# Kernel tuning notes

Measured on AMD Instinct MI355X. Metric: run time of the kernel, lower is better.

The kernel has to match this reference:

```python
import jax, jax.numpy as jnp
import numpy as np

N = 20000      # atoms
E = 240000     # edges (avg degree ~12, matches _AVG_DEGREE_MATPES)
C = 128        # sphere_channels
ZMAX = 100     # max_num_elements
NG = 600       # GaussianSmearing(0, cutoff, 600, 2.0)
CUTOFF = 6.0
WIDTH = 2.0    # basis_width_scalar
RESCALE = 12.0 # _AVG_DEGREE_MATPES
LN_EPS = 1e-5
# xyz -> (y,z,x): real-SH component order for l=1, so Wigner D^(1) = P R P^T
P = np.array([[0.,1.,0.],[0.,0.,1.],[1.,0.,0.]], dtype=np.float32)


def _layernorm(x, g, b):
    mu = jnp.mean(x, axis=-1, keepdims=True)
    var = jnp.mean((x - mu) ** 2, axis=-1, keepdims=True)
    return g * (x - mu) * jax.lax.rsqrt(var + LN_EPS) + b


def init_edge_rot_mat(ev):
    # faithful port of init_edge_rot_mat (torch uses .detach())
    ev = jax.lax.stop_gradient(ev)
    dist = jnp.maximum(jnp.linalg.norm(ev, axis=1, keepdims=True), 1e-8)
    nx = ev / dist
    ref = jnp.eye(3, dtype=ev.dtype)[jnp.argmin(jnp.abs(nx), axis=1)]
    nz = jnp.cross(nx, ref)
    nz = nz / jnp.maximum(jnp.linalg.norm(nz, axis=1, keepdims=True), 1e-8)
    ny = jnp.cross(nx, nz)
    ny = ny / jnp.maximum(jnp.linalg.norm(ny, axis=1, keepdims=True), 1e-8)
    # edge_rot_mat_inv has columns [nz, nx, -ny]; rot = inv^T -> rows [nz, nx, -ny]
    return jnp.stack([nz, nx, -ny], axis=1)  # [E,3,3]


def setup_inputs() -> dict:
    key = jax.random.key(0)
    ks = jax.random.split(key, 10)
    s = 0.02
    return {
        'edge_distance_vec': jax.random.normal(ks[0], (E, 3), jnp.float32) * 2.0,
        'sphere_emb': jax.random.normal(ks[1], (ZMAX, C), jnp.float32) * s,
        'src_emb': jax.random.normal(ks[2], (ZMAX, C), jnp.float32) * s,
        'tgt_emb': jax.random.normal(ks[3], (ZMAX, C), jnp.float32) * s,
        'W1': jax.random.normal(ks[4], (NG + 2 * C, C), jnp.float32) * s,
        'b1': jnp.zeros((C,), jnp.float32),
        'g1': jnp.ones((C,), jnp.float32),
        'be1': jnp.zeros((C,), jnp.float32),
        'W2': jax.random.normal(ks[5], (C, C), jnp.float32) * s,
        'b2': jnp.zeros((C,), jnp.float32),
        'g2': jnp.ones((C,), jnp.float32),
        'be2': jnp.zeros((C,), jnp.float32),
        'W3': jax.random.normal(ks[6], (C, 2 * C), jnp.float32) * s,
        'b3': jnp.zeros((2 * C,), jnp.float32),
        'atomic_numbers': jax.random.randint(ks[7], (N,), 0, ZMAX),
        'edge_index': jax.random.randint(ks[8], (2, E), 0, N),
    }


def reference(edge_distance_vec, sphere_emb, src_emb, tgt_emb,
              W1, b1, g1, be1, W2, b2, g2, be2, W3, b3,
              atomic_numbers, edge_index):
    src, dst = edge_index[0], edge_index[1]
    Pm = jnp.asarray(P)
    # per-edge rotation to edge-aligned frame and its l=1 Wigner matrix
    rot = init_edge_rot_mat(edge_distance_vec)               # [E,3,3]
    D1 = jnp.einsum('ij,ejk,lk->eil', Pm, rot, Pm)           # [E,3,3]
    # Gaussian distance expansion (600 basis fns)
    dist = jnp.linalg.norm(edge_distance_vec, axis=1)        # [E]
    offsets = jnp.linspace(0.0, CUTOFF, NG)
    coeff = -0.5 / (WIDTH * (offsets[1] - offsets[0])) ** 2
    gauss = jnp.exp(coeff * (dist[:, None] - offsets[None, :]) ** 2)  # [E,600]
    # edge features: distance basis + source/target atom embeddings
    x_edge = jnp.concatenate(
        [gauss, src_emb[atomic_numbers[src]], tgt_emb[atomic_numbers[dst]]], axis=1)
    # RadialFunction: Linear->LN->SiLU x2, final Linear -> m=0 coefficients
    h = jax.nn.silu(_layernorm(x_edge @ W1 + b1, g1, be1))
    h = jax.nn.silu(_layernorm(h @ W2 + b2, g2, be2))
    m0 = (h @ W3 + b3).reshape(E, 2, C)   # (l=0,m=0) and (l=1,m=0)
    # rotate back to global frame: blockdiag(1, D1)^T applied to (m0[0]; 0, m0[1], 0)
    l0 = m0[:, 0][:, None, :]                                 # [E,1,C]
    l1 = jnp.einsum('ei,ec->eic', D1[:, 1, :], m0[:, 1])      # (D1^T v)_i with v=(0,a,0)
    msg = jnp.concatenate([l0, l1], axis=1)                   # [E,4,C]
    # scatter-sum messages to target nodes, rescale by avg degree
    x_deg = jnp.zeros((N, 4, C), msg.dtype).at[dst].add(msg) / RESCALE
    # node init: atom embedding into l=0 slot, plus edge-degree embedding
    x = x_deg.at[:, 0].add(sphere_emb[atomic_numbers])
    return x
```

## Files before the change

### kernel.cpp

```cpp
#include <hip/hip_runtime.h>
#include <stdint.h>

#define EE 240000
#define NN 20000
#define NB 4096

typedef __attribute__((ext_vector_type(4))) float f32x4;
typedef __attribute__((ext_vector_type(8))) __bf16 bf16x8;
typedef __attribute__((ext_vector_type(8))) short s16x8;

union V8 { s16x8 s; bf16x8 b; uint4 u; };

static constexpr float GC2 =
    (float)((-0.5 / ((12.0 / 599.0) * (12.0 / 599.0))) * 1.4426950408889634);

__device__ __forceinline__ float b2f(unsigned short u) {
    return __uint_as_float(((unsigned)u) << 16);
}
__device__ __forceinline__ unsigned short f2b(float f) {
    unsigned u = __float_as_uint(f);
    return (unsigned short)((u + 0x7fffu + ((u >> 16) & 1u)) >> 16);
}
__device__ __forceinline__ unsigned cvtpk(float lo, float hi) {
    unsigned r;
    asm("v_cvt_pk_bf16_f32 %0, %1, %2" : "=v"(r) : "v"(lo), "v"(hi));
    return r;
}
__device__ __forceinline__ unsigned short ldc(const void* p, int i, bool isb) {
    return isb ? ((const unsigned short*)p)[i] : f2b(((const float*)p)[i]);
}
__device__ __forceinline__ float ldf(const void* p, int i, bool isb) {
    return isb ? b2f(((const unsigned short*)p)[i]) : ((const float*)p)[i];
}
__device__ __forceinline__ bool probe_isb(const void* g1) {
    return ((const unsigned*)g1)[0] != 0x3F800000u;
}

__device__ __forceinline__ int kperm(int p) {
    int wi = p >> 1;
    return ((wi >> 4) << 5) + (wi & 15) + ((p & 1) << 4);
}

#define PREP_PARAMS_TOTAL (114688 + 16384 + 32768 + 2 * 12800 + 6 * 128 + 256)
#define PB ((PREP_PARAMS_TOTAL + 255) / 256)
#define EB ((EE + 255) / 256)

__global__ void prep_all(const void* ev, const int* __restrict__ an,
                         const int* __restrict__ ei,
                         const void* W1, const void* W2, const void* W3,
                         const void* se, const void* te,
                         const void* b1, const void* g1, const void* be1,
                         const void* b2, const void* g2, const void* be2,
                         const void* b3,
                         unsigned short* __restrict__ W1T,
                         unsigned short* __restrict__ W2T,
                         unsigned short* __restrict__ W3T,
                         unsigned short* __restrict__ SE,
                         unsigned short* __restrict__ TE,
                         unsigned short* __restrict__ vecs,
                         uint4* __restrict__ sedge_u, float4* __restrict__ d1_out,
                         int* __restrict__ deg, int* __restrict__ bhist) {
    bool isb = probe_isb(g1);
    int bid = blockIdx.x;
    if (bid < PB) {
        int t = bid * 256 + threadIdx.x;
        if (t < 114688) {
            int j = t & 7, n = (t >> 3) & 127, kb = t >> 10;
            int k = kb * 8 + j;
            unsigned short v = 0;
            if (k < 600) v = ldc(W1, k * 128 + n, isb);
            else if (k >= 608 && k < 864) v = ldc(W1, (k - 8) * 128 + n, isb);
            W1T[t] = v;
            return;
        }
        t -= 114688;
        if (t < 16384) {
            int j = t & 7, n = (t >> 3) & 127, kb = t >> 10;
            W2T[t] = ldc(W2, kperm(kb * 8 + j) * 128 + n, isb);
            return;
        }
        t -= 16384;
        if (t < 32768) {
            int j = t & 7, n = (t >> 3) & 255, kb = t >> 11;
            W3T[t] = ldc(W3, kperm(kb * 8 + j) * 256 + n, isb);
            return;
        }
        t -= 32768;
        if (t < 12800) { SE[t] = ldc(se, t, isb); return; }
        t -= 12800;
        if (t < 12800) { TE[t] = ldc(te, t, isb); return; }
        t -= 12800;
        if (t < 128) { vecs[t] = ldc(b1, t, isb); return; }
        t -= 128;
        if (t < 128) { vecs[128 + t] = ldc(g1, t, isb); return; }
        t -= 128;
        if (t < 128) { vecs[256 + t] = ldc(be1, t, isb); return; }
        t -= 128;
        if (t < 128) { vecs[384 + t] = ldc(b2, t, isb); return; }
        t -= 128;
        if (t < 128) { vecs[512 + t] = ldc(g2, t, isb); return; }
        t -= 128;
        if (t < 128) { vecs[640 + t] = ldc(be2, t, isb); return; }
        t -= 128;
        if (t < 256) { vecs[768 + t] = ldc(b3, t, isb); return; }
        return;
    }
    int e = (bid - PB) * 256 + threadIdx.x;
    if (e >= EE) return;
    float x = ldf(ev, e * 3 + 0, isb);
    float y = ldf(ev, e * 3 + 1, isb);
    float z = ldf(ev, e * 3 + 2, isb);
    float nrm = sqrtf(x * x + y * y + z * z);
    float dc = fmaxf(nrm, 1e-8f);
    float nx0 = x / dc, nx1 = y / dc, nx2 = z / dc;
    float a0 = fabsf(nx0), a1 = fabsf(nx1), a2 = fabsf(nx2);
    int idx = 0; float mv = a0;
    if (a1 < mv) { idx = 1; mv = a1; }
    if (a2 < mv) { idx = 2; }
    float r0 = (idx == 0) ? 1.f : 0.f;
    float r1 = (idx == 1) ? 1.f : 0.f;
    float r2 = (idx == 2) ? 1.f : 0.f;
    float z0 = nx1 * r2 - nx2 * r1;
    float z1 = nx2 * r0 - nx0 * r2;
    float z2 = nx0 * r1 - nx1 * r0;
    float zn = fmaxf(sqrtf(z0 * z0 + z1 * z1 + z2 * z2), 1e-8f);
    z0 /= zn; z1 /= zn; z2 /= zn;
    float y0 = nx1 * z2 - nx2 * z1;
    float y1 = nx2 * z0 - nx0 * z2;
    float y2 = nx0 * z1 - nx1 * z0;
    float yn = fmaxf(sqrtf(y0 * y0 + y1 * y1 + y2 * y2), 1e-8f);
    y0 /= yn; y1 /= yn; y2 /= yn;
    float4 dv; dv.x = -y1; dv.y = -y2; dv.z = -y0; dv.w = 0.f;
    d1_out[e] = dv;
    int zsv = an[ei[e]];
    int dst = ei[EE + e];
    int zdv = an[dst];
    uint4 su;
    su.x = __float_as_uint(nrm);
    su.y = (unsigned)zsv | ((unsigned)zdv << 16);
    su.z = (unsigned)e;
    su.w = 0;
    sedge_u[e] = su;
    atomicAdd(&deg[dst], 1);
    int b = min(NB - 1, (int)(nrm * 512.0f));
    atomicAdd(&bhist[b], 1);
}

__global__ __launch_bounds__(1024) void scan_all(
    const int* __restrict__ deg, const int* __restrict__ bhist,
    int* __restrict__ row_start, int* __restrict__ cursor, int* __restrict__ bcursor) {
    __shared__ int lds[1024];
    int t = threadIdx.x;
    int base = t * 20;
    int loc[20]; int ls = 0;
#pragma unroll
    for (int j = 0; j < 20; ++j) {
        int i = base + j;
        ls += (i < NN) ? deg[i] : 0;
        loc[j] = ls;
    }
    lds[t] = ls; __syncthreads();
    for (int s = 1; s < 1024; s <<= 1) {
        int v = (t >= s) ? lds[t - s] : 0;
        __syncthreads(); lds[t] += v; __syncthreads();
    }
    int off = lds[t] - ls;
#pragma unroll
    for (int j = 0; j < 20; ++j) {
        int i = base + j;
        if (i < NN) {
            row_start[i + 1] = off + loc[j];
            cursor[i] = off + (j ? loc[j - 1] : 0);
        }
    }
    if (t == 0) row_start[0] = 0;
    __syncthreads();
    int b4 = t * 4;
    int l4[4]; int bs = 0;
#pragma unroll
    for (int j = 0; j < 4; ++j) { bs += bhist[b4 + j]; l4[j] = bs; }
    lds[t] = bs; __syncthreads();
    for (int s = 1; s < 1024; s <<= 1) {
        int v = (t >= s) ? lds[t - s] : 0;
        __syncthreads(); lds[t] += v; __syncthreads();
    }
    int boff = lds[t] - bs;
#pragma unroll
    for (int j = 0; j < 4; ++j) bcursor[b4 + j] = boff + (j ? l4[j - 1] : 0);
}

__global__ void fill_sorted(const int* __restrict__ ei,
                            const uint4* __restrict__ sedge_u,
                            const float4* __restrict__ d1v,
                            int* __restrict__ cursor, int* __restrict__ bcursor,
                            uint4* __restrict__ sedge_s, float4* __restrict__ d1s) {
    int e = blockIdx.x * 256 + threadIdx.x;
    if (e >= EE) return;
    uint4 su = sedge_u[e];
    int dst = ei[EE + e];
    int p = atomicAdd(&cursor[dst], 1);
    float d = __uint_as_float(su.x);
    int b = min(NB - 1, (int)(d * 512.0f));
    int sp = atomicAdd(&bcursor[b], 1);
    su.z = (unsigned)p;
    sedge_s[sp] = su;
    d1s[p] = d1v[e];
}

__device__ __forceinline__ void ln_silu(f32x4 (&acc)[8],
                                        const unsigned short* __restrict__ gamma,
                                        const unsigned short* __restrict__ beta,
                                        int i16, int quad,
                                        unsigned short (*ht)[136]) {
    float gm[8], bt[8];
#pragma unroll
    for (int nt = 0; nt < 8; ++nt) {
        gm[nt] = b2f(gamma[nt * 16 + i16]);
        bt[nt] = b2f(beta[nt * 16 + i16]);
    }
#pragma unroll
    for (int r = 0; r < 4; ++r) {
        float s = 0.f, s2 = 0.f;
#pragma unroll
        for (int nt = 0; nt < 8; ++nt) {
            float v = acc[nt][r];
            s += v; s2 += v * v;
        }
#pragma unroll
        for (int m = 1; m < 16; m <<= 1) {
            s += __shfl_xor(s, m);
            s2 += __shfl_xor(s2, m);
        }
        float mu = s * (1.f / 128.f);
        float var = s2 * (1.f / 128.f) - mu * mu;
        float rs = rsqrtf(var + 1e-5f);
        unsigned* wrow = (unsigned*)ht[quad * 4 + r];
#pragma unroll
        for (int ntp = 0; ntp < 4; ++ntp) {
            float zz[2];
#pragma unroll
            for (int h = 0; h < 2; ++h) {
                int nt = 2 * ntp + h;
                float y = gm[nt] * (acc[nt][r] - mu) * rs + bt[nt];
                zz[h] = y * __builtin_amdgcn_rcpf(1.f + exp2f(-1.4426950409f * y));
            }
            wrow[ntp * 16 + i16] = cvtpk(zz[0], zz[1]);
        }
    }
}

template <bool MSG>
__global__ __launch_bounds__(256, 6) void edge_mlp(
    const unsigned short* __restrict__ W1T, const unsigned short* __restrict__ W2T,
    const unsigned short* __restrict__ W3T,
    const unsigned short* __restrict__ SE, const unsigned short* __restrict__ TE,
    const unsigned short* __restrict__ vecs,
    const uint4* __restrict__ sedge,
    const int* __restrict__ ei, const float4* __restrict__ d1v,
    unsigned* __restrict__ msg, float* __restrict__ xacc) {
    __shared__ __align__(16) unsigned short htile_s[4][16][136];
    int tid = threadIdx.x;
    int wave = tid >> 6, lane = tid & 63;
    int i16 = lane & 15, quad = lane >> 4;
    unsigned short (*ht)[136] = htile_s[wave];
    int mbase = blockIdx.x * 64 + wave * 16;

    uint4 s0 = sedge[mbase + i16];
    float dd = __uint_as_float(s0.x);
    int seo = (int)(s0.y & 0xFFFFu) * 128;
    int teo = (int)(s0.y >> 16) * 128;
    int dpz = (int)s0.z;

    float dmn = dd, dmx = dd;
#pragma unroll
    for (int m = 1; m < 64; m <<= 1) {
        dmn = fminf(dmn, __shfl_xor(dmn, m));
        dmx = fmaxf(dmx, __shfl_xor(dmx, m));
    }
    int klo = (int)floorf((dmn - 0.285f) * (599.0f / 6.0f));
    int khi = (int)ceilf((dmx + 0.285f) * (599.0f / 6.0f));
    int ka = min(max(klo, 0) >> 5, 19);
    int kb = min((min(khi, 607) >> 5) + 1, 19);

    f32x4 acc[8];
#pragma unroll
    for (int nt = 0; nt < 8; ++nt) {
        float b = b2f(vecs[nt * 16 + i16]);
#pragma unroll
        for (int q = 0; q < 4; ++q) acc[nt][q] = b;
    }

#pragma unroll 1
    for (int ks = ka; ks < kb; ++ks) {
        int k0 = ks * 32 + quad * 8;
        float e[8];
#pragma unroll
        for (int j = 0; j < 8; ++j) {
            float t = dd - (float)(k0 + j) * (6.0f / 599.0f);
            e[j] = exp2f(GC2 * t * t);
        }
        V8 af;
        af.u.x = cvtpk(e[0], e[1]);
        af.u.y = cvtpk(e[2], e[3]);
        af.u.z = cvtpk(e[4], e[5]);
        af.u.w = cvtpk(e[6], e[7]);
        const unsigned short* w1p = W1T + (((ks * 4 + quad) * 128 + i16) << 3);
#pragma unroll
        for (int nt = 0; nt < 8; ++nt) {
            V8 bf_; bf_.s = *(const s16x8*)(w1p + nt * 128);
            acc[nt] = __builtin_amdgcn_mfma_f32_16x16x32_bf16(af.b, bf_.b, acc[nt], 0, 0, 0);
        }
    }
#pragma unroll 1
    for (int ks = 19; ks < 27; ++ks) {
        int k0 = ks * 32 + quad * 8;
        V8 af;
        if (ks < 23) af.s = *(const s16x8*)(SE + seo + (k0 - 608));
        else         af.s = *(const s16x8*)(TE + teo + (k0 - 736));
        const unsigned short* w1p = W1T + (((ks * 4 + quad) * 128 + i16) << 3);
#pragma unroll
        for (int nt = 0; nt < 8; ++nt) {
            V8 bf_; bf_.s = *(const s16x8*)(w1p + nt * 128);
            acc[nt] = __builtin_amdgcn_mfma_f32_16x16x32_bf16(af.b, bf_.b, acc[nt], 0, 0, 0);
        }
    }
    ln_silu(acc, vecs + 128, vecs + 256, i16, quad, ht);

#pragma unroll
    for (int nt = 0; nt < 8; ++nt) {
        float b = b2f(vecs[384 + nt * 16 + i16]);
#pragma unroll
        for (int q = 0; q < 4; ++q) acc[nt][q] = b;
    }
#pragma unroll 1
    for (int ks = 0; ks < 4; ++ks) {
        int k0 = ks * 32 + quad * 8;
        V8 a0;
        a0.s = *(const s16x8*)&ht[i16][k0];
        const unsigned short* w2p = W2T + (((ks * 4 + quad) * 128 + i16) << 3);
#pragma unroll
        for (int nt = 0; nt < 8; ++nt) {
            V8 bf_; bf_.s = *(const s16x8*)(w2p + nt * 128);
            acc[nt] = __builtin_amdgcn_mfma_f32_16x16x32_bf16(a0.b, bf_.b, acc[nt], 0, 0, 0);
        }
    }
    ln_silu(acc, vecs + 512, vecs + 640, i16, quad, ht);

#pragma unroll 1
    for (int half = 0; half < 2; ++half) {
#pragma unroll
        for (int nt = 0; nt < 8; ++nt) {
            float b = b2f(vecs[768 + half * 128 + nt * 16 + i16]);
#pragma unroll
            for (int q = 0; q < 4; ++q) acc[nt][q] = b;
        }
#pragma unroll 1
        for (int ks = 0; ks < 4; ++ks) {
            int k0 = ks * 32 + quad * 8;
            V8 a0;
            a0.s = *(const s16x8*)&ht[i16][k0];
            const unsigned short* w3p = W3T + (((ks * 4 + quad) * 256 + half * 128 + i16) << 3);
#pragma unroll
            for (int nt = 0; nt < 8; ++nt) {
                V8 bf_; bf_.s = *(const s16x8*)(w3p + nt * 128);
                acc[nt] = __builtin_amdgcn_mfma_f32_16x16x32_bf16(a0.b, bf_.b, acc[nt], 0, 0, 0);
            }
        }
        if constexpr (MSG) {
#pragma unroll
            for (int r = 0; r < 4; ++r) {
                int dp = __shfl(dpz, quad * 4 + r);
                unsigned* mrow = msg + (size_t)dp * 128 + half * 64 + i16;
#pragma unroll
                for (int ntp = 0; ntp < 4; ++ntp)
                    mrow[ntp * 16] = cvtpk(acc[2 * ntp][r], acc[2 * ntp + 1][r]);
            }
        } else {
#pragma unroll
            for (int r = 0; r < 4; ++r) {
                int eidx = mbase + quad * 4 + r;
                int dn = ei[EE + eidx];
                float* xb = xacc + (size_t)dn * 512;
                if (half == 0) {
#pragma unroll
                    for (int nt = 0; nt < 8; ++nt)
                        atomicAdd(xb + nt * 16 + i16, acc[nt][r]);
                } else {
                    float4 dv = d1v[eidx];
#pragma unroll
                    for (int nt = 0; nt < 8; ++nt) {
                        float val = acc[nt][r];
                        atomicAdd(xb + 128 + nt * 16 + i16, val * dv.x);
                        atomicAdd(xb + 256 + nt * 16 + i16, val * dv.y);
                        atomicAdd(xb + 384 + nt * 16 + i16, val * dv.z);
                    }
                }
            }
        }
    }
}

__global__ __launch_bounds__(256) void gather(
    const unsigned* __restrict__ msg,
    const float4* __restrict__ d1s, const int* __restrict__ row_start,
    const void* __restrict__ sp, const void* __restrict__ g1,
    const int* __restrict__ an, float* __restrict__ out) {
    __shared__ float cbuf[2][8][64];
    int tid = threadIdx.x;
    int w = tid >> 6, l = tid & 63;
    int nl = w >> 1, sub = w & 1;
    int n = blockIdx.x * 2 + nl;
    int c0 = ((l >> 4) << 5) | (l & 15);
    int i0 = row_start[n], i1 = row_start[n + 1];
    float a0 = 0.f, a1 = 0.f, x0 = 0.f, x1 = 0.f,
          y0 = 0.f, y1 = 0.f, z0 = 0.f, z1 = 0.f;
#pragma unroll 2
    for (int i = i0 + sub; i < i1; i += 2) {
        unsigned m0 = msg[(size_t)i * 128 + l];
        unsigned m1 = msg[(size_t)i * 128 + 64 + l];
        float4 dv = d1s[i];
        float p0 = b2f((unsigned short)m0), p1 = b2f((unsigned short)(m0 >> 16));
        float q0 = b2f((unsigned short)m1), q1 = b2f((unsigned short)(m1 >> 16));
        a0 += p0; a1 += p1;
        x0 += q0 * dv.x; x1 += q1 * dv.x;
        y0 += q0 * dv.y; y1 += q1 * dv.y;
        z0 += q0 * dv.z; z1 += q1 * dv.z;
    }
    if (sub) {
        cbuf[nl][0][l] = a0; cbuf[nl][1][l] = a1;
        cbuf[nl][2][l] = x0; cbuf[nl][3][l] = x1;
        cbuf[nl][4][l] = y0; cbuf[nl][5][l] = y1;
        cbuf[nl][6][l] = z0; cbuf[nl][7][l] = z1;
    }
    __syncthreads();
    if (!sub) {
        a0 += cbuf[nl][0][l]; a1 += cbuf[nl][1][l];
        x0 += cbuf[nl][2][l]; x1 += cbuf[nl][3][l];
        y0 += cbuf[nl][4][l]; y1 += cbuf[nl][5][l];
        z0 += cbuf[nl][6][l]; z1 += cbuf[nl][7][l];
        bool isb = probe_isb(g1);
        float* ob = out + (size_t)n * 512;
        int zb = an[n] * 128 + c0;
        constexpr float R = 1.f / 12.f;
        ob[c0]            = a0 * R + ldf(sp, zb, isb);
        ob[c0 + 16]       = a1 * R + ldf(sp, zb + 16, isb);
        ob[128 + c0]      = x0 * R;
        ob[128 + c0 + 16] = x1 * R;
        ob[256 + c0]      = y0 * R;
        ob[256 + c0 + 16] = y1 * R;
        ob[384 + c0]      = z0 * R;
        ob[384 + c0 + 16] = z1 * R;
    }
}

__global__ void finalize(const float* __restrict__ xacc, const void* __restrict__ sp,
                         const void* __restrict__ g1,
                         const int* __restrict__ an, float* __restrict__ out) {
    int t = blockIdx.x * 256 + threadIdx.x;
    bool isb = probe_isb(g1);
    int n = t >> 9, sc = t & 511;
    float v = xacc[t] * (1.f / 12.f);
    if (sc < 128) v += ldf(sp, an[n] * 128 + sc, isb);
    out[t] = v;
}

extern "C" void kernel_launch(void* const* d_in, const int* in_sizes, int n_in,
                              void* d_out, int out_size, void* d_ws, size_t ws_size,
                              hipStream_t stream) {
    const void* ev         = d_in[0];
    const void* sphere_emb = d_in[1];
    const void* src_emb    = d_in[2];
    const void* tgt_emb    = d_in[3];
    const void* W1  = d_in[4];  const void* b1  = d_in[5];
    const void* g1  = d_in[6];  const void* be1 = d_in[7];
    const void* W2  = d_in[8];  const void* b2  = d_in[9];
    const void* g2  = d_in[10]; const void* be2 = d_in[11];
    const void* W3  = d_in[12]; const void* b3  = d_in[13];
    const int* an   = (const int*)d_in[14];
    const int* ei   = (const int*)d_in[15];

    char* ws = (char*)d_ws;
    const size_t NEED_MSG = 132000000;

    if (ws_size >= NEED_MSG) {
        size_t off = 0;
        unsigned* msg = (unsigned*)(ws + off); off += (size_t)EE * 512;
        uint4* sedge_u = (uint4*)(ws + 0);
        float4* d1v    = (float4*)(ws + 3840000);
        float4* d1s    = (float4*)(ws + off);  off += (size_t)EE * 16;
        uint4* sedge_s = (uint4*)(ws + off);   off += (size_t)EE * 16;
        int* deg       = (int*)(ws + off);     off += (size_t)NN * 4;
        int* bhist     = (int*)(ws + off);     off += NB * 4;
        int* row_start = (int*)(ws + off);     off += (size_t)(NN + 4) * 4;
        int* cursor    = (int*)(ws + off);     off += (size_t)NN * 4;
        int* bcursor   = (int*)(ws + off);     off += NB * 4;
        unsigned short* W1T = (unsigned short*)(ws + off); off += 128 * 896 * 2;
        unsigned short* W2T = (unsigned short*)(ws + off); off += 128 * 128 * 2;
        unsigned short* W3T = (unsigned short*)(ws + off); off += 256 * 128 * 2;
        unsigned short* SEc = (unsigned short*)(ws + off); off += 100 * 128 * 2;
        unsigned short* TEc = (unsigned short*)(ws + off); off += 100 * 128 * 2;
        unsigned short* vecs = (unsigned short*)(ws + off); off += 1024 * 2;

        hipMemsetAsync(deg, 0, (size_t)(NN + NB) * 4, stream);
        prep_all<<<PB + EB, 256, 0, stream>>>(
            ev, an, ei, W1, W2, W3, src_emb, tgt_emb,
            b1, g1, be1, b2, g2, be2, b3,
            W1T, W2T, W3T, SEc, TEc, vecs, sedge_u, d1v, deg, bhist);
        scan_all<<<1, 1024, 0, stream>>>(deg, bhist, row_start, cursor, bcursor);
        fill_sorted<<<(EE + 255) / 256, 256, 0, stream>>>(
            ei, sedge_u, d1v, cursor, bcursor, sedge_s, d1s);
        edge_mlp<true><<<EE / 64, 256, 0, stream>>>(
            W1T, W2T, W3T, SEc, TEc, vecs, sedge_s,
            (const int*)nullptr, (const float4*)nullptr, msg, (float*)nullptr);
        gather<<<NN / 2, 256, 0, stream>>>(msg, d1s, row_start,
                                           sphere_emb, g1, an, (float*)d_out);
    } else {
        size_t off = 0;
        float* xacc    = (float*)(ws + off);   off += (size_t)NN * 512 * 4;
        uint4* sedge_u = (uint4*)(ws + off);   off += (size_t)EE * 16;
        float4* d1v    = (float4*)(ws + off);  off += (size_t)EE * 16;
        int* deg       = (int*)(ws + off);     off += (size_t)NN * 4;
        int* bhist     = (int*)(ws + off);     off += NB * 4;
        unsigned short* W1T = (unsigned short*)(ws + off); off += 128 * 896 * 2;
        unsigned short* W2T = (unsigned short*)(ws + off); off += 128 * 128 * 2;
        unsigned short* W3T = (unsigned short*)(ws + off); off += 256 * 128 * 2;
        unsigned short* SEc = (unsigned short*)(ws + off); off += 100 * 128 * 2;
        unsigned short* TEc = (unsigned short*)(ws + off); off += 100 * 128 * 2;
        unsigned short* vecs = (unsigned short*)(ws + off); off += 1024 * 2;

        hipMemsetAsync(xacc, 0, (size_t)NN * 512 * 4, stream);
        hipMemsetAsync(deg, 0, (size_t)(NN + NB) * 4, stream);
        prep_all<<<PB + EB, 256, 0, stream>>>(
            ev, an, ei, W1, W2, W3, src_emb, tgt_emb,
            b1, g1, be1, b2, g2, be2, b3,
            W1T, W2T, W3T, SEc, TEc, vecs, sedge_u, d1v, deg, bhist);
        edge_mlp<false><<<EE / 64, 256, 0, stream>>>(
            W1T, W2T, W3T, SEc, TEc, vecs, sedge_u, ei, d1v,
            (unsigned*)nullptr, xacc);
        finalize<<<(NN * 512) / 256, 256, 0, stream>>>(xacc, sphere_emb, g1, an,
                                                       (float*)d_out);
    }
}
```

Measured before the change: 348.9 us.

## Precompute per-element embedding projections through W1 and widen gather to one node per block

The source/target embedding part of the first linear layer depends only on atomic number, so it is precomputed per element (100x128 for each of src and tgt, with b1 folded into the src table) in prep_all. edge_mlp then initialises its accumulators from these tables and drops eight K-steps of MFMA per tile. This trades per-edge matrix work for a small serial 128-long dot loop per table entry in the prep kernel, which could take a noticeable time. The gather kernel also changes from two nodes per block with two waves each to one node per block with four waves striding over edges, followed by a three-way LDS reduction.

```diff
diff --git a/kernel.cpp b/kernel.cpp
--- a/kernel.cpp
+++ b/kernel.cpp
@@ -41,7 +41,7 @@
     return ((wi >> 4) << 5) + (wi & 15) + ((p & 1) << 4);
 }
 
-#define PREP_PARAMS_TOTAL (114688 + 16384 + 32768 + 2 * 12800 + 6 * 128 + 256)
+#define PREP_PARAMS_TOTAL (77824 + 16384 + 32768 + 6400 + 6400 + 1024)
 #define PB ((PREP_PARAMS_TOTAL + 255) / 256)
 #define EB ((EE + 255) / 256)
 
@@ -55,8 +55,8 @@
                          unsigned short* __restrict__ W1T,
                          unsigned short* __restrict__ W2T,
                          unsigned short* __restrict__ W3T,
-                         unsigned short* __restrict__ SE,
-                         unsigned short* __restrict__ TE,
+                         float2* __restrict__ SEWT,
+                         float2* __restrict__ TEWT,
                          unsigned short* __restrict__ vecs,
                          uint4* __restrict__ sedge_u, float4* __restrict__ d1_out,
                          int* __restrict__ deg, int* __restrict__ bhist) {
@@ -64,16 +64,13 @@
     int bid = blockIdx.x;
     if (bid < PB) {
         int t = bid * 256 + threadIdx.x;
-        if (t < 114688) {
+        if (t < 77824) {
             int j = t & 7, n = (t >> 3) & 127, kb = t >> 10;
             int k = kb * 8 + j;
-            unsigned short v = 0;
-            if (k < 600) v = ldc(W1, k * 128 + n, isb);
-            else if (k >= 608 && k < 864) v = ldc(W1, (k - 8) * 128 + n, isb);
-            W1T[t] = v;
+            W1T[t] = (k < 600) ? ldc(W1, k * 128 + n, isb) : (unsigned short)0;
             return;
         }
-        t -= 114688;
+        t -= 77824;
         if (t < 16384) {
             int j = t & 7, n = (t >> 3) & 127, kb = t >> 10;
             W2T[t] = ldc(W2, kperm(kb * 8 + j) * 128 + n, isb);
@@ -86,10 +83,34 @@
             return;
         }
         t -= 32768;
-        if (t < 12800) { SE[t] = ldc(se, t, isb); return; }
-        t -= 12800;
-        if (t < 12800) { TE[t] = ldc(te, t, isb); return; }
-        t -= 12800;
+        if (t < 6400) {
+            int z = t >> 6, wi = t & 63;
+            int c0 = ((wi >> 4) << 5) | (wi & 15), c1 = c0 + 16;
+            float a0 = ldf(b1, c0, isb), a1 = ldf(b1, c1, isb);
+            for (int k = 0; k < 128; ++k) {
+                float sv = ldf(se, z * 128 + k, isb);
+                a0 += sv * ldf(W1, (600 + k) * 128 + c0, isb);
+                a1 += sv * ldf(W1, (600 + k) * 128 + c1, isb);
+            }
+            float2 w; w.x = a0; w.y = a1;
+            SEWT[t] = w;
+            return;
+        }
+        t -= 6400;
+        if (t < 6400) {
+            int z = t >> 6, wi = t & 63;
+            int c0 = ((wi >> 4) << 5) | (wi & 15), c1 = c0 + 16;
+            float a0 = 0.f, a1 = 0.f;
+            for (int k = 0; k < 128; ++k) {
+                float tv = ldf(te, z * 128 + k, isb);
+                a0 += tv * ldf(W1, (728 + k) * 128 + c0, isb);
+                a1 += tv * ldf(W1, (728 + k) * 128 + c1, isb);
+            }
+            float2 w; w.x = a0; w.y = a1;
+            TEWT[t] = w;
+            return;
+        }
+        t -= 6400;
         if (t < 128) { vecs[t] = ldc(b1, t, isb); return; }
         t -= 128;
         if (t < 128) { vecs[128 + t] = ldc(g1, t, isb); return; }
@@ -253,7 +274,7 @@
 __global__ __launch_bounds__(256, 6) void edge_mlp(
     const unsigned short* __restrict__ W1T, const unsigned short* __restrict__ W2T,
     const unsigned short* __restrict__ W3T,
-    const unsigned short* __restrict__ SE, const unsigned short* __restrict__ TE,
+    const float2* __restrict__ SEWT, const float2* __restrict__ TEWT,
     const unsigned short* __restrict__ vecs,
     const uint4* __restrict__ sedge,
     const int* __restrict__ ei, const float4* __restrict__ d1v,
@@ -267,8 +288,6 @@
 
     uint4 s0 = sedge[mbase + i16];
     float dd = __uint_as_float(s0.x);
-    int seo = (int)(s0.y & 0xFFFFu) * 128;
-    int teo = (int)(s0.y >> 16) * 128;
     int dpz = (int)s0.z;
 
     float dmn = dd, dmx = dd;
@@ -284,10 +303,17 @@
 
     f32x4 acc[8];
 #pragma unroll
-    for (int nt = 0; nt < 8; ++nt) {
-        float b = b2f(vecs[nt * 16 + i16]);
-#pragma unroll
-        for (int q = 0; q < 4; ++q) acc[nt][q] = b;
+    for (int r = 0; r < 4; ++r) {
+        unsigned zy = (unsigned)__shfl((int)s0.y, quad * 4 + r);
+        const float2* sw = SEWT + (zy & 0xFFFFu) * 64 + i16;
+        const float2* tw = TEWT + (zy >> 16) * 64 + i16;
+#pragma unroll
+        for (int ntp = 0; ntp < 4; ++ntp) {
+            float2 a = sw[ntp * 16];
+            float2 b = tw[ntp * 16];
+            acc[2 * ntp][r]     = a.x + b.x;
+            acc[2 * ntp + 1][r] = a.y + b.y;
+        }
     }
 
 #pragma unroll 1
@@ -304,19 +330,6 @@
         af.u.y = cvtpk(e[2], e[3]);
         af.u.z = cvtpk(e[4], e[5]);
         af.u.w = cvtpk(e[6], e[7]);
-        const unsigned short* w1p = W1T + (((ks * 4 + quad) * 128 + i16) << 3);
-#pragma unroll
-        for (int nt = 0; nt < 8; ++nt) {
-            V8 bf_; bf_.s = *(const s16x8*)(w1p + nt * 128);
-            acc[nt] = __builtin_amdgcn_mfma_f32_16x16x32_bf16(af.b, bf_.b, acc[nt], 0, 0, 0);
-        }
-    }
-#pragma unroll 1
-    for (int ks = 19; ks < 27; ++ks) {
-        int k0 = ks * 32 + quad * 8;
-        V8 af;
-        if (ks < 23) af.s = *(const s16x8*)(SE + seo + (k0 - 608));
-        else         af.s = *(const s16x8*)(TE + teo + (k0 - 736));
         const unsigned short* w1p = W1T + (((ks * 4 + quad) * 128 + i16) << 3);
 #pragma unroll
         for (int nt = 0; nt < 8; ++nt) {
@@ -405,17 +418,15 @@
     const float4* __restrict__ d1s, const int* __restrict__ row_start,
     const void* __restrict__ sp, const void* __restrict__ g1,
     const int* __restrict__ an, float* __restrict__ out) {
-    __shared__ float cbuf[2][8][64];
+    __shared__ float cbuf[3][8][64];
     int tid = threadIdx.x;
-    int w = tid >> 6, l = tid & 63;
-    int nl = w >> 1, sub = w & 1;
-    int n = blockIdx.x * 2 + nl;
+    int sub = tid >> 6, l = tid & 63;
+    int n = blockIdx.x;
     int c0 = ((l >> 4) << 5) | (l & 15);
     int i0 = row_start[n], i1 = row_start[n + 1];
     float a0 = 0.f, a1 = 0.f, x0 = 0.f, x1 = 0.f,
           y0 = 0.f, y1 = 0.f, z0 = 0.f, z1 = 0.f;
-#pragma unroll 2
-    for (int i = i0 + sub; i < i1; i += 2) {
+    for (int i = i0 + sub; i < i1; i += 4) {
         unsigned m0 = msg[(size_t)i * 128 + l];
         unsigned m1 = msg[(size_t)i * 128 + 64 + l];
         float4 dv = d1s[i];
@@ -427,17 +438,20 @@
         z0 += q0 * dv.z; z1 += q1 * dv.z;
     }
     if (sub) {
-        cbuf[nl][0][l] = a0; cbuf[nl][1][l] = a1;
-        cbuf[nl][2][l] = x0; cbuf[nl][3][l] = x1;
-        cbuf[nl][4][l] = y0; cbuf[nl][5][l] = y1;
-        cbuf[nl][6][l] = z0; cbuf[nl][7][l] = z1;
+        cbuf[sub - 1][0][l] = a0; cbuf[sub - 1][1][l] = a1;
+        cbuf[sub - 1][2][l] = x0; cbuf[sub - 1][3][l] = x1;
+        cbuf[sub - 1][4][l] = y0; cbuf[sub - 1][5][l] = y1;
+        cbuf[sub - 1][6][l] = z0; cbuf[sub - 1][7][l] = z1;
     }
     __syncthreads();
     if (!sub) {
-        a0 += cbuf[nl][0][l]; a1 += cbuf[nl][1][l];
-        x0 += cbuf[nl][2][l]; x1 += cbuf[nl][3][l];
-        y0 += cbuf[nl][4][l]; y1 += cbuf[nl][5][l];
-        z0 += cbuf[nl][6][l]; z1 += cbuf[nl][7][l];
+#pragma unroll
+        for (int q = 0; q < 3; ++q) {
+            a0 += cbuf[q][0][l]; a1 += cbuf[q][1][l];
+            x0 += cbuf[q][2][l]; x1 += cbuf[q][3][l];
+            y0 += cbuf[q][4][l]; y1 += cbuf[q][5][l];
+            z0 += cbuf[q][6][l]; z1 += cbuf[q][7][l];
+        }
         bool isb = probe_isb(g1);
         float* ob = out + (size_t)n * 512;
         int zb = an[n] * 128 + c0;
@@ -494,26 +508,26 @@
         int* row_start = (int*)(ws + off);     off += (size_t)(NN + 4) * 4;
         int* cursor    = (int*)(ws + off);     off += (size_t)NN * 4;
         int* bcursor   = (int*)(ws + off);     off += NB * 4;
-        unsigned short* W1T = (unsigned short*)(ws + off); off += 128 * 896 * 2;
+        unsigned short* W1T = (unsigned short*)(ws + off); off += 77824 * 2;
         unsigned short* W2T = (unsigned short*)(ws + off); off += 128 * 128 * 2;
         unsigned short* W3T = (unsigned short*)(ws + off); off += 256 * 128 * 2;
-        unsigned short* SEc = (unsigned short*)(ws + off); off += 100 * 128 * 2;
-        unsigned short* TEc = (unsigned short*)(ws + off); off += 100 * 128 * 2;
+        float2* SEWT   = (float2*)(ws + off);  off += 6400 * 8;
+        float2* TEWT   = (float2*)(ws + off);  off += 6400 * 8;
         unsigned short* vecs = (unsigned short*)(ws + off); off += 1024 * 2;
 
         hipMemsetAsync(deg, 0, (size_t)(NN + NB) * 4, stream);
         prep_all<<<PB + EB, 256, 0, stream>>>(
             ev, an, ei, W1, W2, W3, src_emb, tgt_emb,
             b1, g1, be1, b2, g2, be2, b3,
-            W1T, W2T, W3T, SEc, TEc, vecs, sedge_u, d1v, deg, bhist);
+            W1T, W2T, W3T, SEWT, TEWT, vecs, sedge_u, d1v, deg, bhist);
         scan_all<<<1, 1024, 0, stream>>>(deg, bhist, row_start, cursor, bcursor);
         fill_sorted<<<(EE + 255) / 256, 256, 0, stream>>>(
             ei, sedge_u, d1v, cursor, bcursor, sedge_s, d1s);
         edge_mlp<true><<<EE / 64, 256, 0, stream>>>(
-            W1T, W2T, W3T, SEc, TEc, vecs, sedge_s,
+            W1T, W2T, W3T, SEWT, TEWT, vecs, sedge_s,
             (const int*)nullptr, (const float4*)nullptr, msg, (float*)nullptr);
-        gather<<<NN / 2, 256, 0, stream>>>(msg, d1s, row_start,
-                                           sphere_emb, g1, an, (float*)d_out);
+        gather<<<NN, 256, 0, stream>>>(msg, d1s, row_start,
+                                       sphere_emb, g1, an, (float*)d_out);
     } else {
         size_t off = 0;
         float* xacc    = (float*)(ws + off);   off += (size_t)NN * 512 * 4;
@@ -521,11 +535,11 @@
         float4* d1v    = (float4*)(ws + off);  off += (size_t)EE * 16;
         int* deg       = (int*)(ws + off);     off += (size_t)NN * 4;
         int* bhist     = (int*)(ws + off);     off += NB * 4;
-        unsigned short* W1T = (unsigned short*)(ws + off); off += 128 * 896 * 2;
+        unsigned short* W1T = (unsigned short*)(ws + off); off += 77824 * 2;
         unsigned short* W2T = (unsigned short*)(ws + off); off += 128 * 128 * 2;
         unsigned short* W3T = (unsigned short*)(ws + off); off += 256 * 128 * 2;
-        unsigned short* SEc = (unsigned short*)(ws + off); off += 100 * 128 * 2;
-        unsigned short* TEc = (unsigned short*)(ws + off); off += 100 * 128 * 2;
+        float2* SEWT   = (float2*)(ws + off);  off += 6400 * 8;
+        float2* TEWT   = (float2*)(ws + off);  off += 6400 * 8;
         unsigned short* vecs = (unsigned short*)(ws + off); off += 1024 * 2;
 
         hipMemsetAsync(xacc, 0, (size_t)NN * 512 * 4, stream);
@@ -533,9 +547,9 @@
         prep_all<<<PB + EB, 256, 0, stream>>>(
             ev, an, ei, W1, W2, W3, src_emb, tgt_emb,
             b1, g1, be1, b2, g2, be2, b3,
-            W1T, W2T, W3T, SEc, TEc, vecs, sedge_u, d1v, deg, bhist);
+            W1T, W2T, W3T, SEWT, TEWT, vecs, sedge_u, d1v, deg, bhist);
         edge_mlp<false><<<EE / 64, 256, 0, stream>>>(
-            W1T, W2T, W3T, SEc, TEc, vecs, sedge_u, ei, d1v,
+            W1T, W2T, W3T, SEWT, TEWT, vecs, sedge_u, ei, d1v,
             (unsigned*)nullptr, xacc);
         finalize<<<(NN * 512) / 256, 256, 0, stream>>>(xacc, sphere_emb, g1, an,
                                                        (float*)d_out);
```

Result: no change. 352.3 us (+1.0%).
